# Performance work log

Hardware: AMD Instinct MI355X
Metric: run time of the kernel (lower is better)

Reference implementation:

```python
import jax, jax.numpy as jnp
import numpy as np

B, S, D = 4, 4096, 256


def setup_inputs() -> dict:
    key = jax.random.key(0)
    ks = jax.random.split(key, 8)
    inv = 1.0 / np.sqrt(D)
    return {
        "input_tensor": jax.random.normal(ks[0], (B, S, D), dtype=jnp.float32),
        "attention_mask": jax.random.randint(ks[1], (B, S, S), 0, 2) == 1,
        "Wq": jax.random.uniform(ks[2], (D, D), jnp.float32, -inv, inv),
        "bq": jax.random.uniform(ks[3], (D,), jnp.float32, -inv, inv),
        "Wk": jax.random.uniform(ks[4], (D, D), jnp.float32, -inv, inv),
        "bk": jax.random.uniform(ks[5], (D,), jnp.float32, -inv, inv),
        "Wv": jax.random.uniform(ks[6], (D, D), jnp.float32, -inv, inv),
        "bv": jax.random.uniform(ks[7], (D,), jnp.float32, -inv, inv),
    }


def reference(input_tensor, attention_mask, Wq, bq, Wk, bk, Wv, bv):
    # Linear projections: y = x @ W.T + b  (nn.Linear convention, W is [out,in])
    query = jnp.einsum("bsd,ed->bse", input_tensor, Wq) + bq
    key = jnp.einsum("bsd,ed->bse", input_tensor, Wk) + bk
    value = jnp.einsum("bsd,ed->bse", input_tensor, Wv) + bv
    # Faithful quirk: original scales by sqrt(query.size(1)) == sqrt(seq_len)
    scale = jnp.asarray(query.shape[1], query.dtype) ** 0.5
    scores = jnp.einsum("bqd,bkd->bqk", query, key) / scale  # [B,S,S]
    scores = jnp.where(attention_mask, jnp.asarray(-1e9, scores.dtype), scores)
    attn = jax.nn.softmax(scores, axis=-1)
    # dropout with p=0.0 is identity (eval-mode reference)
    context = jnp.einsum("bqk,bkd->bqd", attn, value)
    return context
```

## Files before the change

### kernel.cpp

```cpp
#include <hip/hip_runtime.h>
#include <hip/hip_bf16.h>
#include <stdint.h>

#define BB 4
#define SS 4096
#define DD 256

typedef __attribute__((ext_vector_type(4))) float f32x4;
typedef __attribute__((ext_vector_type(8))) short s16x8;

__device__ __forceinline__ ushort f2bf(float f) {
  __hip_bfloat16 h = __float2bfloat16(f);
  return __builtin_bit_cast(ushort, h);
}

__global__ void convert_kernel(const float* __restrict__ X,
                               const float* __restrict__ Wq,
                               const float* __restrict__ Wk,
                               const float* __restrict__ Wv,
                               const float* __restrict__ bq,
                               const float* __restrict__ bk,
                               const float* __restrict__ bv,
                               ushort* __restrict__ Xb,
                               ushort* __restrict__ Wb,
                               float* __restrict__ bias) {
  int tid = blockIdx.x * blockDim.x + threadIdx.x;
  int stride = gridDim.x * blockDim.x;
  const int NX4 = (BB * SS * DD) / 4;
  for (int i = tid; i < NX4; i += stride) {
    float4 v = ((const float4*)X)[i];
    ushort4 o = { f2bf(v.x), f2bf(v.y), f2bf(v.z), f2bf(v.w) };
    ((ushort4*)Xb)[i] = o;
  }
  const int NW4 = (DD * DD) / 4;
  for (int i = tid; i < NW4; i += stride) {
    float4 a = ((const float4*)Wq)[i];
    float4 b = ((const float4*)Wk)[i];
    float4 c = ((const float4*)Wv)[i];
    ushort4 oa = { f2bf(a.x), f2bf(a.y), f2bf(a.z), f2bf(a.w) };
    ushort4 ob = { f2bf(b.x), f2bf(b.y), f2bf(b.z), f2bf(b.w) };
    ushort4 oc = { f2bf(c.x), f2bf(c.y), f2bf(c.z), f2bf(c.w) };
    ((ushort4*)Wb)[i]           = oa;
    ((ushort4*)Wb)[NW4 + i]     = ob;
    ((ushort4*)Wb)[2 * NW4 + i] = oc;
  }
  if (tid < DD) {
    bias[tid]          = bq[tid];
    bias[DD + tid]     = bk[tid];
    bias[2 * DD + tid] = bv[tid];
  }
}

#define LROW 40

__global__ __launch_bounds__(256) void proj_gemm(const ushort* __restrict__ Xb,
                                                 const ushort* __restrict__ Wb,
                                                 const float* __restrict__ bias,
                                                 ushort* __restrict__ Qb,
                                                 ushort* __restrict__ Kb,
                                                 ushort* __restrict__ Vt) {
  __shared__ ushort Al[128 * LROW];
  __shared__ ushort Bl[128 * LROW];
  const int m0 = blockIdx.x * 128;
  const int n0 = blockIdx.y * 128;
  const int t = threadIdx.x;
  const int lane = t & 63;
  const int w = t >> 6;
  const int wr = w & 1, wc = w >> 1;
  const int col = lane & 15;
  const int quad = lane >> 4;

  f32x4 acc[4][4];
#pragma unroll
  for (int i = 0; i < 4; i++)
#pragma unroll
    for (int j = 0; j < 4; j++) acc[i][j] = f32x4{0.f, 0.f, 0.f, 0.f};

  const int ci0 = t, ci1 = 256 + t;
  const int r0 = ci0 >> 2, c0 = ci0 & 3;
  const int r1 = ci1 >> 2, c1 = ci1 & 3;

  s16x8 pa0 = *(const s16x8*)(Xb + (m0 + r0) * DD + c0 * 8);
  s16x8 pa1 = *(const s16x8*)(Xb + (m0 + r1) * DD + c1 * 8);
  s16x8 pb0 = *(const s16x8*)(Wb + (n0 + r0) * DD + c0 * 8);
  s16x8 pb1 = *(const s16x8*)(Wb + (n0 + r1) * DD + c1 * 8);

  for (int kk = 0; kk < DD; kk += 32) {
    __syncthreads();
    *(s16x8*)&Al[r0 * LROW + c0 * 8] = pa0;
    *(s16x8*)&Al[r1 * LROW + c1 * 8] = pa1;
    *(s16x8*)&Bl[r0 * LROW + c0 * 8] = pb0;
    *(s16x8*)&Bl[r1 * LROW + c1 * 8] = pb1;
    __syncthreads();
    const int kn = kk + 32;
    if (kn < DD) {
      pa0 = *(const s16x8*)(Xb + (m0 + r0) * DD + kn + c0 * 8);
      pa1 = *(const s16x8*)(Xb + (m0 + r1) * DD + kn + c1 * 8);
      pb0 = *(const s16x8*)(Wb + (n0 + r0) * DD + kn + c0 * 8);
      pb1 = *(const s16x8*)(Wb + (n0 + r1) * DD + kn + c1 * 8);
    }
    s16x8 af[4], bfr[4];
#pragma unroll
    for (int mi = 0; mi < 4; mi++)
      af[mi] = *(const s16x8*)&Al[(wr * 64 + mi * 16 + col) * LROW + quad * 8];
#pragma unroll
    for (int ni = 0; ni < 4; ni++)
      bfr[ni] = *(const s16x8*)&Bl[(wc * 64 + ni * 16 + col) * LROW + quad * 8];
#pragma unroll
    for (int mi = 0; mi < 4; mi++)
#pragma unroll
      for (int ni = 0; ni < 4; ni++)
        acc[mi][ni] = __builtin_amdgcn_mfma_f32_16x16x32_bf16(af[mi], bfr[ni], acc[mi][ni], 0, 0, 0);
  }

  const int region = n0 >> 8;
#pragma unroll
  for (int mi = 0; mi < 4; mi++) {
    const int gm = m0 + wr * 64 + mi * 16 + quad * 4;
#pragma unroll
    for (int ni = 0; ni < 4; ni++) {
      const int gn = n0 + wc * 64 + ni * 16 + col;
      const float bb = bias[gn];
      f32x4 v = acc[mi][ni];
      if (region == 0) {
#pragma unroll
        for (int rg = 0; rg < 4; rg++)
          Qb[(gm + rg) * DD + gn] = f2bf((v[rg] + bb) * 0.015625f);
      } else if (region == 1) {
        const int d = gn - 256;
#pragma unroll
        for (int rg = 0; rg < 4; rg++)
          Kb[(gm + rg) * DD + d] = f2bf(v[rg] + bb);
      } else {
        const int d = gn - 512;
        const int b = gm >> 12;
        const int s = gm & (SS - 1);
        ushort4 o = { f2bf(v[0] + bb), f2bf(v[1] + bb), f2bf(v[2] + bb), f2bf(v[3] + bb) };
        *(ushort4*)&Vt[((size_t)(b << 8) + d) * SS + s] = o;
      }
    }
  }
}

#define NKT 32
#define KROW 264
#define VROW 40
#define PROW 40

#define KL_U (NKT * KROW)
#define VL_U (DD * VROW)
#define PL_U (16 * PROW)
#define VOFF (2 * KL_U)
#define POFF (VOFF + 2 * VL_U)
#define SM_U (POFF + 8 * PL_U)

#define XSTRIDE 72

__global__ __launch_bounds__(512) void attn_kernel(const ushort* __restrict__ Qb,
                                                   const ushort* __restrict__ Kb,
                                                   const ushort* __restrict__ Vt,
                                                   const int* __restrict__ mask,
                                                   float* __restrict__ out) {
  __shared__ __align__(16) ushort sm[SM_U];

  const int qt = blockIdx.x;
  const int b = blockIdx.y;
  const int t = threadIdx.x;
  const int g = t >> 8;
  const int tg = t & 255;
  const int lane = t & 63;
  const int w = tg >> 6;
  const int w8 = t >> 6;
  const int col = lane & 15;
  const int quad = lane >> 4;

  ushort* Kl = sm + g * KL_U;
  ushort* Vl = sm + VOFF + g * VL_U;
  ushort* Pw = sm + POFF + w8 * PL_U;

  const int q0 = qt * 64;
  const int qrow = q0 + w * 16;

  s16x8 qf[8];
  {
    const ushort* qp = Qb + ((size_t)b * SS + qrow + col) * DD + quad * 8;
#pragma unroll
    for (int dc = 0; dc < 8; dc++) qf[dc] = *(const s16x8*)(qp + dc * 32);
  }

  int kr[4], kc[4], vd[4], vc[4];
#pragma unroll
  for (int i = 0; i < 4; i++) {
    const int ci = i * 256 + tg;
    kr[i] = ci >> 5; kc[i] = ci & 31;
    vd[i] = ci >> 2; vc[i] = ci & 3;
  }

  const ushort* Kg = Kb + (size_t)b * SS * DD;
  const ushort* Vg = Vt + (size_t)b * DD * SS;
  const int* Mg = mask + ((size_t)b * SS + qrow + quad * 4) * SS;

  f32x4 Oc[16];
#pragma unroll
  for (int i = 0; i < 16; i++) Oc[i] = f32x4{0.f, 0.f, 0.f, 0.f};
  float m_i[4] = {-INFINITY, -INFINITY, -INFINITY, -INFINITY};
  float l_i[4] = {0.f, 0.f, 0.f, 0.f};

  const int NT2 = (SS / NKT) / 2;
  const int kb0 = g * NT2 * NKT;

  s16x8 pk[4], pv[4];
  int pm[2][4];
#pragma unroll
  for (int i = 0; i < 4; i++) {
    pk[i] = *(const s16x8*)(Kg + (size_t)(kb0 + kr[i]) * DD + kc[i] * 8);
    pv[i] = *(const s16x8*)(Vg + (size_t)vd[i] * SS + kb0 + vc[i] * 8);
  }
#pragma unroll
  for (int jt = 0; jt < 2; jt++)
#pragma unroll
    for (int rg = 0; rg < 4; rg++) pm[jt][rg] = Mg[rg * SS + kb0 + jt * 16 + col];

  for (int tt = 0; tt < NT2; tt++) {
    __syncthreads();
#pragma unroll
    for (int i = 0; i < 4; i++) {
      *(s16x8*)&Kl[kr[i] * KROW + kc[i] * 8] = pk[i];
      *(s16x8*)&Vl[vd[i] * VROW + vc[i] * 8] = pv[i];
    }
    __syncthreads();
    int mcur[2][4];
#pragma unroll
    for (int jt = 0; jt < 2; jt++)
#pragma unroll
      for (int rg = 0; rg < 4; rg++) mcur[jt][rg] = pm[jt][rg];
    if (tt + 1 < NT2) {
      const int k0n = kb0 + (tt + 1) * NKT;
#pragma unroll
      for (int i = 0; i < 4; i++) {
        pk[i] = *(const s16x8*)(Kg + ((size_t)k0n + kr[i]) * DD + kc[i] * 8);
        pv[i] = *(const s16x8*)(Vg + (size_t)vd[i] * SS + k0n + vc[i] * 8);
      }
#pragma unroll
      for (int jt = 0; jt < 2; jt++)
#pragma unroll
        for (int rg = 0; rg < 4; rg++) pm[jt][rg] = Mg[rg * SS + k0n + jt * 16 + col];
    }

    f32x4 st[2];
    __builtin_amdgcn_s_setprio(1);
#pragma unroll
    for (int jt = 0; jt < 2; jt++) {
      f32x4 s = f32x4{0.f, 0.f, 0.f, 0.f};
#pragma unroll
      for (int dc = 0; dc < 8; dc++) {
        s16x8 kb = *(const s16x8*)&Kl[(jt * 16 + col) * KROW + dc * 32 + quad * 8];
        s = __builtin_amdgcn_mfma_f32_16x16x32_bf16(qf[dc], kb, s, 0, 0, 0);
      }
      st[jt] = s;
    }
    __builtin_amdgcn_s_setprio(0);
#pragma unroll
    for (int jt = 0; jt < 2; jt++)
#pragma unroll
      for (int rg = 0; rg < 4; rg++)
        if (mcur[jt][rg]) st[jt][rg] = -1e9f;

    float al[4];
#pragma unroll
    for (int rg = 0; rg < 4; rg++) {
      float v = fmaxf(st[0][rg], st[1][rg]);
      v = fmaxf(v, __shfl_xor(v, 1));
      v = fmaxf(v, __shfl_xor(v, 2));
      v = fmaxf(v, __shfl_xor(v, 4));
      v = fmaxf(v, __shfl_xor(v, 8));
      const float mn = fmaxf(m_i[rg], v);
      al[rg] = __expf(m_i[rg] - mn);
      m_i[rg] = mn;
    }
#pragma unroll
    for (int rg = 0; rg < 4; rg++) {
      const float p0 = __expf(st[0][rg] - m_i[rg]);
      const float p1 = __expf(st[1][rg] - m_i[rg]);
      st[0][rg] = p0; st[1][rg] = p1;
      float s2 = p0 + p1;
      s2 += __shfl_xor(s2, 1);
      s2 += __shfl_xor(s2, 2);
      s2 += __shfl_xor(s2, 4);
      s2 += __shfl_xor(s2, 8);
      l_i[rg] = l_i[rg] * al[rg] + s2;
    }
#pragma unroll
    for (int dt = 0; dt < 16; dt++)
#pragma unroll
      for (int rg = 0; rg < 4; rg++) Oc[dt][rg] *= al[rg];

#pragma unroll
    for (int jt = 0; jt < 2; jt++)
#pragma unroll
      for (int rg = 0; rg < 4; rg++)
        Pw[(quad * 4 + rg) * PROW + jt * 16 + col] = f2bf(st[jt][rg]);
    s16x8 pa = *(const s16x8*)&Pw[col * PROW + quad * 8];

    __builtin_amdgcn_s_setprio(1);
#pragma unroll
    for (int dt = 0; dt < 16; dt++) {
      s16x8 vb = *(const s16x8*)&Vl[(dt * 16 + col) * VROW + quad * 8];
      Oc[dt] = __builtin_amdgcn_mfma_f32_16x16x32_bf16(pa, vb, Oc[dt], 0, 0, 0);
    }
    __builtin_amdgcn_s_setprio(0);
  }

  __syncthreads();
  float* ex = (float*)sm;
  float* slot = ex + (size_t)(w * 64 + lane) * XSTRIDE;
  if (g == 1) {
#pragma unroll
    for (int rg = 0; rg < 4; rg++) { slot[rg] = m_i[rg]; slot[4 + rg] = l_i[rg]; }
#pragma unroll
    for (int dt = 0; dt < 16; dt++) *(f32x4*)&slot[8 + dt * 4] = Oc[dt];
  }
  __syncthreads();
  if (g == 0) {
    float a0[4], a1[4], inv[4];
#pragma unroll
    for (int rg = 0; rg < 4; rg++) {
      const float m1 = slot[rg];
      const float l1 = slot[4 + rg];
      const float mm = fmaxf(m_i[rg], m1);
      a0[rg] = __expf(m_i[rg] - mm);
      a1[rg] = __expf(m1 - mm);
      inv[rg] = 1.0f / (l_i[rg] * a0[rg] + l1 * a1[rg]);
    }
    float* op = out + ((size_t)b * SS + qrow + quad * 4) * DD;
#pragma unroll
    for (int dt = 0; dt < 16; dt++) {
      const f32x4 o1 = *(const f32x4*)&slot[8 + dt * 4];
#pragma unroll
      for (int rg = 0; rg < 4; rg++)
        op[rg * DD + dt * 16 + col] = (Oc[dt][rg] * a0[rg] + o1[rg] * a1[rg]) * inv[rg];
    }
  }
}

extern "C" void kernel_launch(void* const* d_in, const int* in_sizes, int n_in,
                              void* d_out, int out_size, void* d_ws, size_t ws_size,
                              hipStream_t stream) {
  const float* X  = (const float*)d_in[0];
  const int* mask = (const int*)d_in[1];
  const float* Wq = (const float*)d_in[2];
  const float* bq = (const float*)d_in[3];
  const float* Wk = (const float*)d_in[4];
  const float* bk = (const float*)d_in[5];
  const float* Wv = (const float*)d_in[6];
  const float* bv = (const float*)d_in[7];
  float* out = (float*)d_out;

  ushort* base = (ushort*)d_ws;
  ushort* Xb = base;
  ushort* Wb = Xb + (size_t)BB * SS * DD;
  ushort* Qb = Wb + (size_t)3 * DD * DD;
  ushort* Kb = Qb + (size_t)BB * SS * DD;
  ushort* Vt = Kb + (size_t)BB * SS * DD;
  float* bias = (float*)(Vt + (size_t)BB * SS * DD);

  convert_kernel<<<1024, 256, 0, stream>>>(X, Wq, Wk, Wv, bq, bk, bv, Xb, Wb, bias);
  proj_gemm<<<dim3(128, 6), 256, 0, stream>>>(Xb, Wb, bias, Qb, Kb, Vt);
  attn_kernel<<<dim3(64, 4), 512, 0, stream>>>(Qb, Kb, Vt, mask, out);
}
```

Measured before the change: 524.3 us.

## Split attention KV range four ways per block with 1024-thread blocks

The attention kernel now runs four 256-thread groups per block, each covering a quarter of the key sequence, where before two groups each covered half. Partial softmax states are merged pairwise through shared memory in two reduction stages. LDS row padding is also changed (KROW/VROW/PROW/XSTRIDE). The goal is more waves in flight to hide memory latency, since the grid has only 256 blocks. The cost is more LDS per block, an extra merge stage with more barriers, and possible new bank conflicts from the changed padding.

New measurement: 1.417 ms. 170% more time.

```diff
diff --git a/kernel.cpp b/kernel.cpp
--- a/kernel.cpp
+++ b/kernel.cpp
@@ -143,24 +143,24 @@
 }
 
 #define NKT 32
-#define KROW 264
-#define VROW 40
-#define PROW 40
+#define KROW 260
+#define VROW 36
+#define PROW 36
 
 #define KL_U (NKT * KROW)
 #define VL_U (DD * VROW)
 #define PL_U (16 * PROW)
-#define VOFF (2 * KL_U)
-#define POFF (VOFF + 2 * VL_U)
-#define SM_U (POFF + 8 * PL_U)
-
-#define XSTRIDE 72
-
-__global__ __launch_bounds__(512) void attn_kernel(const ushort* __restrict__ Qb,
-                                                   const ushort* __restrict__ Kb,
-                                                   const ushort* __restrict__ Vt,
-                                                   const int* __restrict__ mask,
-                                                   float* __restrict__ out) {
+#define VOFF (4 * KL_U)
+#define POFF (VOFF + 4 * VL_U)
+#define SM_U (POFF + 16 * PL_U)
+
+#define XSTRIDE 76
+
+__global__ __launch_bounds__(1024) void attn_kernel(const ushort* __restrict__ Qb,
+                                                    const ushort* __restrict__ Kb,
+                                                    const ushort* __restrict__ Vt,
+                                                    const int* __restrict__ mask,
+                                                    float* __restrict__ out) {
   __shared__ __align__(16) ushort sm[SM_U];
 
   const int qt = blockIdx.x;
@@ -170,13 +170,13 @@
   const int tg = t & 255;
   const int lane = t & 63;
   const int w = tg >> 6;
-  const int w8 = t >> 6;
+  const int w16 = t >> 6;
   const int col = lane & 15;
   const int quad = lane >> 4;
 
   ushort* Kl = sm + g * KL_U;
   ushort* Vl = sm + VOFF + g * VL_U;
-  ushort* Pw = sm + POFF + w8 * PL_U;
+  ushort* Pw = sm + POFF + w16 * PL_U;
 
   const int q0 = qt * 64;
   const int qrow = q0 + w * 16;
@@ -206,8 +206,8 @@
   float m_i[4] = {-INFINITY, -INFINITY, -INFINITY, -INFINITY};
   float l_i[4] = {0.f, 0.f, 0.f, 0.f};
 
-  const int NT2 = (SS / NKT) / 2;
-  const int kb0 = g * NT2 * NKT;
+  const int NT4 = (SS / NKT) / 4;
+  const int kb0 = g * NT4 * NKT;
 
   s16x8 pk[4], pv[4];
   int pm[2][4];
@@ -221,7 +221,7 @@
 #pragma unroll
     for (int rg = 0; rg < 4; rg++) pm[jt][rg] = Mg[rg * SS + kb0 + jt * 16 + col];
 
-  for (int tt = 0; tt < NT2; tt++) {
+  for (int tt = 0; tt < NT4; tt++) {
     __syncthreads();
 #pragma unroll
     for (int i = 0; i < 4; i++) {
@@ -234,7 +234,7 @@
     for (int jt = 0; jt < 2; jt++)
 #pragma unroll
       for (int rg = 0; rg < 4; rg++) mcur[jt][rg] = pm[jt][rg];
-    if (tt + 1 < NT2) {
+    if (tt + 1 < NT4) {
       const int k0n = kb0 + (tt + 1) * NKT;
 #pragma unroll
       for (int i = 0; i < 4; i++) {
@@ -311,10 +311,40 @@
     __builtin_amdgcn_s_setprio(0);
   }
 
+  float* ex = (float*)sm;
   __syncthreads();
-  float* ex = (float*)sm;
-  float* slot = ex + (size_t)(w * 64 + lane) * XSTRIDE;
-  if (g == 1) {
+  if (g & 1) {
+    float* slot = ex + (size_t)((g >> 1) * 256 + w * 64 + lane) * XSTRIDE;
+#pragma unroll
+    for (int rg = 0; rg < 4; rg++) { slot[rg] = m_i[rg]; slot[4 + rg] = l_i[rg]; }
+#pragma unroll
+    for (int dt = 0; dt < 16; dt++) *(f32x4*)&slot[8 + dt * 4] = Oc[dt];
+  }
+  __syncthreads();
+  if (!(g & 1)) {
+    const float* slot = ex + (size_t)((g >> 1) * 256 + w * 64 + lane) * XSTRIDE;
+    float a0[4], a1[4];
+#pragma unroll
+    for (int rg = 0; rg < 4; rg++) {
+      const float m1 = slot[rg];
+      const float l1 = slot[4 + rg];
+      const float mm = fmaxf(m_i[rg], m1);
+      a0[rg] = __expf(m_i[rg] - mm);
+      a1[rg] = __expf(m1 - mm);
+      m_i[rg] = mm;
+      l_i[rg] = l_i[rg] * a0[rg] + l1 * a1[rg];
+    }
+#pragma unroll
+    for (int dt = 0; dt < 16; dt++) {
+      const f32x4 o1 = *(const f32x4*)&slot[8 + dt * 4];
+#pragma unroll
+      for (int rg = 0; rg < 4; rg++)
+        Oc[dt][rg] = Oc[dt][rg] * a0[rg] + o1[rg] * a1[rg];
+    }
+  }
+  __syncthreads();
+  if (g == 2) {
+    float* slot = ex + (size_t)(w * 64 + lane) * XSTRIDE;
 #pragma unroll
     for (int rg = 0; rg < 4; rg++) { slot[rg] = m_i[rg]; slot[4 + rg] = l_i[rg]; }
 #pragma unroll
@@ -322,6 +352,7 @@
   }
   __syncthreads();
   if (g == 0) {
+    const float* slot = ex + (size_t)(w * 64 + lane) * XSTRIDE;
     float a0[4], a1[4], inv[4];
 #pragma unroll
     for (int rg = 0; rg < 4; rg++) {
@@ -366,5 +397,5 @@
 
   convert_kernel<<<1024, 256, 0, stream>>>(X, Wq, Wk, Wv, bq, bk, bv, Xb, Wb, bias);
   proj_gemm<<<dim3(128, 6), 256, 0, stream>>>(Xb, Wb, bias, Qb, Kb, Vt);
-  attn_kernel<<<dim3(64, 4), 512, 0, stream>>>(Qb, Kb, Vt, mask, out);
+  attn_kernel<<<dim3(64, 4), 1024, 0, stream>>>(Qb, Kb, Vt, mask, out);
 }
```

## Split attention KV range across two grid slices and merge partials in a second kernel

Applied to the files above, without the earlier changes.

The attention grid gains a z dimension of 2, so each block processes half of the key range (split-K / flash-decoding style). This doubles the block count from 256 to 512 so more of the GPU's compute units are occupied. Each slice writes unnormalized partial outputs plus per-row max and sum, and a new merge kernel combines the two slices and normalizes. LDS row padding is also reduced, which changes bank-conflict behaviour. The cost is extra global traffic for the partial outputs and one more kernel launch.

Result: slower. 948.7 us (+80.9%).

```diff
diff --git a/kernel.cpp b/kernel.cpp
--- a/kernel.cpp
+++ b/kernel.cpp
@@ -143,9 +143,9 @@
 }
 
 #define NKT 32
-#define KROW 264
-#define VROW 40
-#define PROW 40
+#define KROW 260
+#define VROW 36
+#define PROW 36
 
 #define KL_U (NKT * KROW)
 #define VL_U (DD * VROW)
@@ -160,11 +160,14 @@
                                                    const ushort* __restrict__ Kb,
                                                    const ushort* __restrict__ Vt,
                                                    const int* __restrict__ mask,
-                                                   float* __restrict__ out) {
+                                                   float* __restrict__ out,
+                                                   float* __restrict__ O1,
+                                                   float* __restrict__ Ml) {
   __shared__ __align__(16) ushort sm[SM_U];
 
   const int qt = blockIdx.x;
   const int b = blockIdx.y;
+  const int z = blockIdx.z;
   const int t = threadIdx.x;
   const int g = t >> 8;
   const int tg = t & 255;
@@ -206,8 +209,8 @@
   float m_i[4] = {-INFINITY, -INFINITY, -INFINITY, -INFINITY};
   float l_i[4] = {0.f, 0.f, 0.f, 0.f};
 
-  const int NT2 = (SS / NKT) / 2;
-  const int kb0 = g * NT2 * NKT;
+  const int NT2 = 1024 / NKT;
+  const int kb0 = z * 2048 + g * 1024;
 
   s16x8 pk[4], pv[4];
   int pm[2][4];
@@ -322,7 +325,7 @@
   }
   __syncthreads();
   if (g == 0) {
-    float a0[4], a1[4], inv[4];
+    float a0[4], a1[4];
 #pragma unroll
     for (int rg = 0; rg < 4; rg++) {
       const float m1 = slot[rg];
@@ -330,17 +333,43 @@
       const float mm = fmaxf(m_i[rg], m1);
       a0[rg] = __expf(m_i[rg] - mm);
       a1[rg] = __expf(m1 - mm);
-      inv[rg] = 1.0f / (l_i[rg] * a0[rg] + l1 * a1[rg]);
-    }
-    float* op = out + ((size_t)b * SS + qrow + quad * 4) * DD;
+      m_i[rg] = mm;
+      l_i[rg] = l_i[rg] * a0[rg] + l1 * a1[rg];
+    }
+    float* op = (z ? O1 : out) + ((size_t)b * SS + qrow + quad * 4) * DD;
 #pragma unroll
     for (int dt = 0; dt < 16; dt++) {
       const f32x4 o1 = *(const f32x4*)&slot[8 + dt * 4];
 #pragma unroll
       for (int rg = 0; rg < 4; rg++)
-        op[rg * DD + dt * 16 + col] = (Oc[dt][rg] * a0[rg] + o1[rg] * a1[rg]) * inv[rg];
-    }
-  }
+        op[rg * DD + dt * 16 + col] = Oc[dt][rg] * a0[rg] + o1[rg] * a1[rg];
+    }
+    if (col == 0) {
+      float2* pml = (float2*)Ml + (size_t)z * BB * SS + (size_t)b * SS + qrow + quad * 4;
+#pragma unroll
+      for (int rg = 0; rg < 4; rg++) pml[rg] = make_float2(m_i[rg], l_i[rg]);
+    }
+  }
+}
+
+__global__ __launch_bounds__(256) void merge_kernel(const float* __restrict__ Ml,
+                                                    const float* __restrict__ O1,
+                                                    float* __restrict__ out) {
+  const int row = blockIdx.x * 4 + (threadIdx.x >> 6);
+  const int lane = threadIdx.x & 63;
+  const float2 ml0 = ((const float2*)Ml)[row];
+  const float2 ml1 = ((const float2*)Ml)[BB * SS + row];
+  const float mm = fmaxf(ml0.x, ml1.x);
+  const float a0 = __expf(ml0.x - mm);
+  const float a1 = __expf(ml1.x - mm);
+  const float inv = 1.0f / (ml0.y * a0 + ml1.y * a1);
+  f32x4* po = (f32x4*)out + (size_t)row * 64 + lane;
+  const f32x4 o0 = *po;
+  const f32x4 o1 = ((const f32x4*)O1)[(size_t)row * 64 + lane];
+  f32x4 r;
+#pragma unroll
+  for (int j = 0; j < 4; j++) r[j] = (o0[j] * a0 + o1[j] * a1) * inv;
+  *po = r;
 }
 
 extern "C" void kernel_launch(void* const* d_in, const int* in_sizes, int n_in,
@@ -363,8 +392,11 @@
   ushort* Kb = Qb + (size_t)BB * SS * DD;
   ushort* Vt = Kb + (size_t)BB * SS * DD;
   float* bias = (float*)(Vt + (size_t)BB * SS * DD);
+  float* O1 = bias + 768;
+  float* Ml = O1 + (size_t)BB * SS * DD;
 
   convert_kernel<<<1024, 256, 0, stream>>>(X, Wq, Wk, Wv, bq, bk, bv, Xb, Wb, bias);
   proj_gemm<<<dim3(128, 6), 256, 0, stream>>>(Xb, Wb, bias, Qb, Kb, Vt);
-  attn_kernel<<<dim3(64, 4), 512, 0, stream>>>(Qb, Kb, Vt, mask, out);
-}
+  attn_kernel<<<dim3(64, 4, 2), 512, 0, stream>>>(Qb, Kb, Vt, mask, out, O1, Ml);
+  merge_kernel<<<(BB * SS) / 4, 256, 0, stream>>>(Ml, O1, out);
+}
```
